# Performance work log

Hardware: AMD Instinct MI355X
Metric: run time of the kernel (lower is better)

The kernel has to match this reference:

```python
import jax, jax.numpy as jnp
import numpy as np

V, D, L, H, T_BLK, DFF = 50257, 768, 12, 12, 1024, 4096
DK = D // H
LN_EPS = 1e-5


def setup_inputs() -> dict:
    key = jax.random.key(0)
    ks = jax.random.split(key, 16)
    s = 0.02
    inp = {
        "idx": jax.random.randint(ks[0], (2, 1024), 0, V),
        "tok_emb": jax.random.normal(ks[1], (V, D), jnp.float32) * s,
        "pos_emb": jax.random.normal(ks[2], (1, T_BLK, D), jnp.float32) * s,
        "ln1_w": jnp.ones((L, D), jnp.float32),
        "ln1_b": jnp.zeros((L, D), jnp.float32),
        "qkv_w": jax.random.normal(ks[3], (L, 3 * D, D), jnp.float32) * s,
        "qkv_b": jnp.zeros((L, 3 * D), jnp.float32),
        "proj_w": jax.random.normal(ks[4], (L, D, D), jnp.float32) * s,
        "proj_b": jnp.zeros((L, D), jnp.float32),
        "ln2_w": jnp.ones((L, D), jnp.float32),
        "ln2_b": jnp.zeros((L, D), jnp.float32),
        "ff1_w": jax.random.normal(ks[5], (L, DFF, D), jnp.float32) * s,
        "ff1_b": jnp.zeros((L, DFF), jnp.float32),
        "ff2_w": jax.random.normal(ks[6], (L, D, DFF), jnp.float32) * s,
        "ff2_b": jnp.zeros((L, D), jnp.float32),
        "lnf_w": jnp.ones((D,), jnp.float32),
        "lnf_b": jnp.zeros((D,), jnp.float32),
        "head_w": jax.random.normal(ks[7], (V, D), jnp.float32) * s,
    }
    return inp


def _layernorm(x, w, b):
    mu = jnp.mean(x, axis=-1, keepdims=True)
    var = jnp.var(x, axis=-1, keepdims=True)
    return (x - mu) * jax.lax.rsqrt(var + LN_EPS) * w + b


def _gpt_forward(idx, tok_emb, pos_emb, ln1_w, ln1_b, qkv_w, qkv_b, proj_w, proj_b,
                 ln2_w, ln2_b, ff1_w, ff1_b, ff2_w, ff2_b, lnf_w, lnf_b, head_w):
    B, T = idx.shape
    x = tok_emb[idx] + pos_emb[:, :T, :]  # [B,T,D]
    mask = jnp.tril(jnp.ones((T, T), bool))  # causal
    scale = 1.0 / np.sqrt(DK)

    def step(x, p):
        l1w, l1b, qw, qb, pw, pb, l2w, l2b, f1w, f1b, f2w, f2b = p
        h = _layernorm(x, l1w, l1b)
        qkv = h @ qw.T + qb  # [B,T,3D]
        q, k, v = jnp.split(qkv, 3, axis=-1)
        q = q.reshape(B, T, H, DK).transpose(0, 2, 1, 3)  # [B,H,T,DK]
        k = k.reshape(B, T, H, DK).transpose(0, 2, 1, 3)
        v = v.reshape(B, T, H, DK).transpose(0, 2, 1, 3)
        att = jnp.einsum('bhtd,bhsd->bhts', q, k) * scale
        att = jnp.where(mask, att, -jnp.inf)
        att = jax.nn.softmax(att, axis=-1)
        y = jnp.einsum('bhts,bhsd->bhtd', att, v)
        y = y.transpose(0, 2, 1, 3).reshape(B, T, D)
        x = x + y @ pw.T + pb
        h2 = _layernorm(x, l2w, l2b)
        ff = jax.nn.gelu(h2 @ f1w.T + f1b, approximate=False) @ f2w.T + f2b
        return x + ff, None

    params = (ln1_w, ln1_b, qkv_w, qkv_b, proj_w, proj_b,
              ln2_w, ln2_b, ff1_w, ff1_b, ff2_w, ff2_b)
    x, _ = jax.lax.scan(step, x, params)
    x = _layernorm(x, lnf_w, lnf_b)
    return x @ head_w.T  # [B,T,V] logits


def reference(idx, tok_emb, pos_emb, ln1_w, ln1_b, qkv_w, qkv_b, proj_w, proj_b,
              ln2_w, ln2_b, ff1_w, ff1_b, ff2_w, ff2_b, lnf_w, lnf_b, head_w):
    return _gpt_forward(idx, tok_emb, pos_emb, ln1_w, ln1_b, qkv_w, qkv_b, proj_w,
                        proj_b, ln2_w, ln2_b, ff1_w, ff1_b, ff2_w, ff2_b,
                        lnf_w, lnf_b, head_w)
```

## Files before the change

kernel.cpp:

```cpp
#include <hip/hip_runtime.h>
#include <hip/hip_bf16.h>
#include <math.h>

#define Dm 768
#define Tt 1024
#define Bb 2
#define Hh 12
#define DFF 4096
#define Ll 12
#define Vv 50257
#define ROWS (Bb*Tt)
#define LN_EPS 1e-5f

typedef unsigned int uint;
typedef unsigned short ushort;
typedef float f32x4 __attribute__((ext_vector_type(4)));
typedef short bf16x8 __attribute__((ext_vector_type(8)));
typedef ushort us8 __attribute__((ext_vector_type(8)));

__device__ __forceinline__ ushort f2bf(float f) {
  uint u = __builtin_bit_cast(uint, f);
  u += 0x7FFFu + ((u >> 16) & 1u);
  return (ushort)(u >> 16);
}

#define GLL(gp, lp)                                                          \
  __builtin_amdgcn_global_load_lds(                                          \
      (const __attribute__((address_space(1))) uint*)(gp),                   \
      (__attribute__((address_space(3))) uint*)(lp), 16, 0, 0)

__global__ __launch_bounds__(256) void embed_ln(
    const int* __restrict__ idx, const float* __restrict__ tok,
    const float* __restrict__ pos, const float* __restrict__ w,
    const float* __restrict__ b, float* __restrict__ x,
    ushort* __restrict__ out) {
  const int row = blockIdx.x;
  const int t = row & (Tt - 1);
  const int tid = threadIdx.x;
  const float* tsrc = tok + (size_t)idx[row] * Dm;
  const float* psrc = pos + (size_t)t * Dm;
  float v[3];
  float sum = 0.f, sq = 0.f;
#pragma unroll
  for (int i = 0; i < 3; i++) {
    const int d = tid + i * 256;
    v[i] = tsrc[d] + psrc[d];
    x[(size_t)row * Dm + d] = v[i];
    sum += v[i]; sq += v[i] * v[i];
  }
#pragma unroll
  for (int off = 32; off > 0; off >>= 1) {
    sum += __shfl_xor(sum, off);
    sq  += __shfl_xor(sq, off);
  }
  __shared__ float red[8];
  const int wid = tid >> 6, lane = tid & 63;
  if (lane == 0) { red[wid] = sum; red[wid + 4] = sq; }
  __syncthreads();
  sum = red[0] + red[1] + red[2] + red[3];
  sq  = red[4] + red[5] + red[6] + red[7];
  const float mu = sum * (1.f / Dm);
  const float var = sq * (1.f / Dm) - mu * mu;
  const float rstd = rsqrtf(var + LN_EPS);
  ushort* dst = out + (size_t)row * Dm;
#pragma unroll
  for (int i = 0; i < 3; i++) {
    const int d = tid + i * 256;
    dst[d] = f2bf((v[i] - mu) * rstd * w[d] + b[d]);
  }
}

__global__ __launch_bounds__(256) void red_ln(
    const float* __restrict__ part, int nsk, const float* __restrict__ bias,
    float* __restrict__ x, const float* __restrict__ w,
    const float* __restrict__ b, ushort* __restrict__ out) {
  const int row = blockIdx.x;
  const int tid = threadIdx.x;
  float v[3];
  float sum = 0.f, sq = 0.f;
#pragma unroll
  for (int i = 0; i < 3; i++) {
    const int d = tid + i * 256;
    const size_t off = (size_t)row * Dm + d;
    float s = x[off] + bias[d];
    for (int k = 0; k < nsk; k++) s += part[(size_t)k * ROWS * Dm + off];
    x[off] = s;
    v[i] = s;
    sum += s; sq += s * s;
  }
#pragma unroll
  for (int off = 32; off > 0; off >>= 1) {
    sum += __shfl_xor(sum, off);
    sq  += __shfl_xor(sq, off);
  }
  __shared__ float red[8];
  const int wid = tid >> 6, lane = tid & 63;
  if (lane == 0) { red[wid] = sum; red[wid + 4] = sq; }
  __syncthreads();
  sum = red[0] + red[1] + red[2] + red[3];
  sq  = red[4] + red[5] + red[6] + red[7];
  const float mu = sum * (1.f / Dm);
  const float var = sq * (1.f / Dm) - mu * mu;
  const float rstd = rsqrtf(var + LN_EPS);
  ushort* dst = out + (size_t)row * Dm;
#pragma unroll
  for (int i = 0; i < 3; i++) {
    const int d = tid + i * 256;
    dst[d] = f2bf((v[i] - mu) * rstd * w[d] + b[d]);
  }
}

__global__ __launch_bounds__(256) void convert_w(
    const float* __restrict__ s, ushort* __restrict__ d, int n4) {
  const int stride = gridDim.x * 256;
  for (int i = blockIdx.x * 256 + threadIdx.x; i < n4; i += stride) {
    const float4 v = ((const float4*)s)[i];
    ushort4 o;
    o.x = f2bf(v.x); o.y = f2bf(v.y); o.z = f2bf(v.z); o.w = f2bf(v.w);
    ((ushort4*)d)[i] = o;
  }
}

#define EPI_QKV 0
#define EPI_PART 1
#define EPI_BIAS_GELU 2
#define EPI_NONE 3

template <int EPI>
__global__ __launch_bounds__(256) void gemm_mfma(
    const ushort* __restrict__ A, const ushort* __restrict__ B,
    const float* __restrict__ bias, void* __restrict__ Cv,
    void* __restrict__ Cv2, int Kloop, int Kstr, int Nloc, int ldC) {
  __shared__ char lds[32768];
  const int tid = threadIdx.x;
  const int l = tid & 63;
  const int wid = __builtin_amdgcn_readfirstlane(tid >> 6);
  const int wr = wid >> 1, wc = wid & 1;
  const int m0 = blockIdx.y * 128;
  const int n0 = blockIdx.x * 128;
  const int z = (EPI == EPI_PART) ? blockIdx.z : 0;
  if (EPI == EPI_PART) { A += (size_t)z * Kloop; B += (size_t)z * Kloop; }

  const int cperm = (((l & 3) ^ ((l >> 3) & 3)) * 8);
  const ushort* gA = A + (size_t)(m0 + wid * 32 + (l >> 2)) * Kstr + cperm;
  int rB = n0 + wid * 32 + (l >> 2);
  rB = min(rB, Nloc - 1);
  const ushort* gB = B + (size_t)rB * Kstr + cperm;

  const int rdSw = (l & 15) * 64 + (((l >> 4) ^ ((l >> 1) & 3)) * 16);
  const int aRd = wr * 4096 + rdSw;
  const int bRd = 8192 + wc * 4096 + rdSw;

  f32x4 acc[4][4] = {};
  const int nt = Kloop / 32;

  {
    const int lb = wid * 2048;
    GLL(gA, lds + lb);          GLL(gA + 16 * Kstr, lds + lb + 1024);
    GLL(gB, lds + 8192 + lb);   GLL(gB + 16 * Kstr, lds + 8192 + lb + 1024);
  }

  for (int t = 0; t < nt; ++t) {
    __syncthreads();
    if (t + 1 < nt) {
      const int base = ((t + 1) & 1) * 16384;
      const int lb = base + wid * 2048;
      const ushort* a = gA + (t + 1) * 32;
      const ushort* b = gB + (t + 1) * 32;
      GLL(a, lds + lb);         GLL(a + 16 * Kstr, lds + lb + 1024);
      GLL(b, lds + 8192 + lb);  GLL(b + 16 * Kstr, lds + 8192 + lb + 1024);
    }
    const int base = (t & 1) * 16384;
    bf16x8 av[4], bv[4];
#pragma unroll
    for (int i = 0; i < 4; ++i) {
      av[i] = *(const bf16x8*)(lds + base + aRd + i * 1024);
      bv[i] = *(const bf16x8*)(lds + base + bRd + i * 1024);
    }
#pragma unroll
    for (int i = 0; i < 4; ++i)
#pragma unroll
      for (int j = 0; j < 4; ++j)
        acc[i][j] = __builtin_amdgcn_mfma_f32_16x16x32_bf16(
            av[i], bv[j], acc[i][j], 0, 0, 0);
  }

#pragma unroll
  for (int fm = 0; fm < 4; ++fm) {
    const int row0 = m0 + wr * 64 + fm * 16 + (l >> 4) * 4;
#pragma unroll
    for (int fn = 0; fn < 4; ++fn) {
      const int col = n0 + wc * 64 + fn * 16 + (l & 15);
      if (col >= Nloc) continue;
      float bi = 0.f;
      if (EPI == EPI_QKV || EPI == EPI_BIAS_GELU) bi = bias[col];
      if (EPI == EPI_QKV && col >= 2 * Dm) {
        const int hh = (col - 2 * Dm) >> 6, dd = col & 63;
        const int bI = row0 >> 10, t0 = row0 & (Tt - 1);
        ushort4 o4;
        o4.x = f2bf(acc[fm][fn][0] + bi);
        o4.y = f2bf(acc[fm][fn][1] + bi);
        o4.z = f2bf(acc[fm][fn][2] + bi);
        o4.w = f2bf(acc[fm][fn][3] + bi);
        *(ushort4*)((ushort*)Cv2 +
                    ((size_t)((bI * Hh + hh) * 64 + dd)) * Tt + t0) = o4;
        continue;
      }
#pragma unroll
      for (int r = 0; r < 4; ++r) {
        float v = acc[fm][fn][r] + bi;
        const size_t off = (size_t)(row0 + r) * ldC + col;
        if (EPI == EPI_BIAS_GELU) {
          v = 0.5f * v * (1.f + erff(v * 0.70710678118654752f));
          ((ushort*)Cv)[off] = f2bf(v);
        } else if (EPI == EPI_QKV) {
          ((ushort*)Cv)[off] = f2bf(v);
        } else if (EPI == EPI_PART) {
          ((float*)Cv)[(size_t)z * ROWS * ldC + off] = v;
        } else {
          ((float*)Cv)[off] = v;
        }
      }
    }
  }
}

__global__ __launch_bounds__(512, 2) void gemm_head8(
    const ushort* __restrict__ A, const ushort* __restrict__ B,
    float* __restrict__ C) {
  __shared__ char lds[131072];
  const int tid = threadIdx.x;
  const int l = tid & 63;
  const int wid = __builtin_amdgcn_readfirstlane(tid >> 6);
  const int wm = wid >> 2, wn = wid & 3;

  const int bid = blockIdx.x;
  const int swz = (bid & 7) * 197 + (bid >> 3);
  const int pan = swz >> 3, mrw = swz & 7;
  const int m0 = mrw * 256;
  const int n0 = pan * 256;

  const ushort* gA[2];
  const ushort* gB[2];
#pragma unroll
  for (int j = 0; j < 2; j++) {
    const int c = tid + j * 512;
    const int r = c >> 2, kq = c & 3;
    gA[j] = A + (size_t)(m0 + r) * Dm + ((kq ^ ((r >> 1) & 3)) * 8);
    int rb = n0 + r;
    rb = min(rb, Vv - 1);
    gB[j] = B + (size_t)rb * Dm + ((kq ^ ((r >> 1) & 3)) * 8);
  }

#define HSTAGE(t)                                                            \
  do {                                                                       \
    char* _lb = lds + ((t) & 3) * 32768;                                     \
    const int _o = (t) * 32;                                                 \
    GLL(gA[0] + _o, _lb + tid * 16);                                         \
    GLL(gA[1] + _o, _lb + 8192 + tid * 16);                                  \
    GLL(gB[0] + _o, _lb + 16384 + tid * 16);                                 \
    GLL(gB[1] + _o, _lb + 24576 + tid * 16);                                 \
  } while (0)

  f32x4 acc[8][4] = {};
  const int s = l & 15, g = l >> 4;

  int aOff[8], bOff[4];
#pragma unroll
  for (int fm = 0; fm < 8; fm++) {
    const int r = wm * 128 + fm * 16 + s;
    aOff[fm] = r * 64 + ((g ^ ((r >> 1) & 3)) * 16);
  }
#pragma unroll
  for (int fn = 0; fn < 4; fn++) {
    const int r = wn * 64 + fn * 16 + s;
    bOff[fn] = 16384 + r * 64 + ((g ^ ((r >> 1) & 3)) * 16);
  }

  HSTAGE(0); HSTAGE(1); HSTAGE(2);
  asm volatile("s_waitcnt vmcnt(8)" ::: "memory");
  __builtin_amdgcn_s_barrier();
  __builtin_amdgcn_sched_barrier(0);

#define HITER(t, VC)                                                         \
  {                                                                          \
    if ((t) + 3 < 24) HSTAGE((t) + 3);                                       \
    char* bb = lds + ((t) & 3) * 32768;                                      \
    bf16x8 av[8], bv[4];                                                     \
    _Pragma("unroll")                                                        \
    for (int fm = 0; fm < 8; fm++) av[fm] = *(const bf16x8*)(bb + aOff[fm]); \
    _Pragma("unroll")                                                        \
    for (int fn = 0; fn < 4; fn++) bv[fn] = *(const bf16x8*)(bb + bOff[fn]); \
    __builtin_amdgcn_s_setprio(1);                                           \
    _Pragma("unroll")                                                        \
    for (int fm = 0; fm < 8; fm++)                                           \
      _Pragma("unroll")                                                      \
      for (int fn = 0; fn < 4; fn++)                                         \
        acc[fm][fn] = __builtin_amdgcn_mfma_f32_16x16x32_bf16(               \
            av[fm], bv[fn], acc[fm][fn], 0, 0, 0);                           \
    __builtin_amdgcn_s_setprio(0);                                           \
    asm volatile("s_waitcnt lgkmcnt(0)" ::: "memory");                       \
    asm volatile("s_waitcnt vmcnt(" #VC ")" ::: "memory");                   \
    __builtin_amdgcn_s_barrier();                                            \
    __builtin_amdgcn_sched_barrier(0);                                       \
  }

#pragma unroll 1
  for (int t = 0; t <= 20; ++t) HITER(t, 8);
  HITER(21, 4);
  HITER(22, 0);
  HITER(23, 0);

#pragma unroll
  for (int fm = 0; fm < 8; ++fm) {
    const int row0 = m0 + wm * 128 + fm * 16 + g * 4;
#pragma unroll
    for (int fn = 0; fn < 4; ++fn) {
      const int col = n0 + wn * 64 + fn * 16 + s;
      if (col >= Vv) continue;
#pragma unroll
      for (int r = 0; r < 4; ++r)
        C[(size_t)(row0 + r) * Vv + col] = acc[fm][fn][r];
    }
  }
}

__global__ __launch_bounds__(128) void attn_mfma(
    const ushort* __restrict__ qkv, const ushort* __restrict__ vTg,
    ushort* __restrict__ y) {
  __shared__ char lds[36864];
  const int tid = threadIdx.x;
  const int l = tid & 63;
  const int w = tid >> 6;
  const int s = l & 15, g = l >> 4;
  const int bq = gridDim.x - 1 - blockIdx.x;
  const int h = blockIdx.y, b = blockIdx.z;
  const int bh = b * Hh + h;

  const int qrow = bq * 32 + w * 16 + s;
  const ushort* qp = qkv + (size_t)(b * Tt + qrow) * 2304 + h * 64 + g * 8;
  const bf16x8 aq0 = *(const bf16x8*)qp;
  const bf16x8 aq1 = *(const bf16x8*)(qp + 32);

  size_t gofs[8];
#pragma unroll
  for (int i = 0; i < 8; i++) {
    const int c = tid + i * 128;
    if (i < 4) {
      const int kr = c >> 3;
      gofs[i] = (size_t)(b * Tt + kr) * 2304 + Dm + h * 64 + ((c & 7) ^ (kr & 7)) * 8;
    } else {
      const int cv = c - 512;
      const int vr = cv >> 3;
      gofs[i] = (size_t)(bh * 64 + vr) * Tt + ((cv & 7) ^ (vr & 7)) * 8;
    }
  }

#define ASTAGE(kt, base)                                                     \
  do {                                                                       \
    _Pragma("unroll")                                                        \
    for (int i = 0; i < 8; i++) {                                            \
      const ushort* p = (i < 4) ? (qkv + gofs[i] + (size_t)(kt) * 147456)    \
                                : (vTg + gofs[i] + (kt) * 64);               \
      GLL(p, lds + (base) + tid * 16 + i * 2048);                            \
    }                                                                        \
  } while (0)

  f32x4 oc[4] = {};
  float mrun[4], lrun[4];
#pragma unroll
  for (int r = 0; r < 4; r++) { mrun[r] = -INFINITY; lrun[r] = 0.f; }

  const int pB = 32768 + w * 2048;
  const int kSw = (s & 7);
  const int nkt = (bq >> 1) + 1;

  ASTAGE(0, 0);
  for (int kt = 0; kt < nkt; ++kt) {
    __syncthreads();
    if (kt + 1 < nkt) ASTAGE(kt + 1, ((kt + 1) & 1) * 16384);
    const int cur = (kt & 1) * 16384;

    f32x4 sc[4];
    __builtin_amdgcn_s_setprio(1);
#pragma unroll
    for (int jn = 0; jn < 4; jn++) {
      const int krow = cur + (jn * 16 + s) * 128;
      const bf16x8 bk0 = *(const bf16x8*)(lds + krow + ((g ^ kSw) * 16));
      const bf16x8 bk1 = *(const bf16x8*)(lds + krow + (((4 + g) ^ kSw) * 16));
      f32x4 z = {};
      z = __builtin_amdgcn_mfma_f32_16x16x32_bf16(aq0, bk0, z, 0, 0, 0);
      z = __builtin_amdgcn_mfma_f32_16x16x32_bf16(aq1, bk1, z, 0, 0, 0);
      sc[jn] = z;
    }
    __builtin_amdgcn_s_setprio(0);

    float cr[4];
    const bool diag = (kt == nkt - 1);
#pragma unroll
    for (int r = 0; r < 4; r++) {
      const int rowg = bq * 32 + w * 16 + g * 4 + r;
      float v[4];
#pragma unroll
      for (int jn = 0; jn < 4; jn++) {
        v[jn] = sc[jn][r] * 0.125f;
        if (diag && (kt * 64 + jn * 16 + s) > rowg) v[jn] = -INFINITY;
      }
      float mx = fmaxf(fmaxf(v[0], v[1]), fmaxf(v[2], v[3]));
      mx = fmaxf(mx, __shfl_xor(mx, 1));
      mx = fmaxf(mx, __shfl_xor(mx, 2));
      mx = fmaxf(mx, __shfl_xor(mx, 4));
      mx = fmaxf(mx, __shfl_xor(mx, 8));
      const float mnew = fmaxf(mrun[r], mx);
      const float corr = __expf(mrun[r] - mnew);
      mrun[r] = mnew;
      float ps = 0.f;
#pragma unroll
      for (int jn = 0; jn < 4; jn++) {
        const float p = __expf(v[jn] - mnew);
        ps += p;
        *(ushort*)(lds + pB + (g * 4 + r) * 128 +
                   (((2 * jn + (s >> 3)) ^ g) * 16) + (s & 7) * 2) = f2bf(p);
      }
      ps += __shfl_xor(ps, 1);
      ps += __shfl_xor(ps, 2);
      ps += __shfl_xor(ps, 4);
      ps += __shfl_xor(ps, 8);
      lrun[r] = lrun[r] * corr + ps;
      cr[r] = corr;
    }

    const float c01 = (s & 1) ? cr[1] : cr[0];
    const float c23 = (s & 1) ? cr[3] : cr[2];
    const float csel = (s & 2) ? c23 : c01;
    const float ccol = __shfl(csel, ((s >> 2) << 4) | s);
#pragma unroll
    for (int fm = 0; fm < 4; fm++) {
      oc[fm][0] *= ccol; oc[fm][1] *= ccol;
      oc[fm][2] *= ccol; oc[fm][3] *= ccol;
    }

    const bf16x8 bp0 = *(const bf16x8*)(lds + pB + s * 128 + ((g ^ (s >> 2)) * 16));
    const bf16x8 bp1 = *(const bf16x8*)(lds + pB + s * 128 + (((4 + g) ^ (s >> 2)) * 16));
    __builtin_amdgcn_s_setprio(1);
#pragma unroll
    for (int fm = 0; fm < 4; fm++) {
      const int vrow = cur + 8192 + (fm * 16 + s) * 128;
      const bf16x8 av0 = *(const bf16x8*)(lds + vrow + ((g ^ kSw) * 16));
      const bf16x8 av1 = *(const bf16x8*)(lds + vrow + (((4 + g) ^ kSw) * 16));
      oc[fm] = __builtin_amdgcn_mfma_f32_16x16x32_bf16(av0, bp0, oc[fm], 0, 0, 0);
      oc[fm] = __builtin_amdgcn_mfma_f32_16x16x32_bf16(av1, bp1, oc[fm], 0, 0, 0);
    }
    __builtin_amdgcn_s_setprio(0);
  }

  float li[4];
#pragma unroll
  for (int r = 0; r < 4; r++) li[r] = 1.f / lrun[r];
  const float l01 = (s & 1) ? li[1] : li[0];
  const float l23 = (s & 1) ? li[3] : li[2];
  const float lsel = (s & 2) ? l23 : l01;
  const float lcol = __shfl(lsel, ((s >> 2) << 4) | s);
  ushort* yp = y + (size_t)(b * Tt + qrow) * Dm + h * 64;
#pragma unroll
  for (int fm = 0; fm < 4; fm++) {
    ushort4 o4;
    o4.x = f2bf(oc[fm][0] * lcol);
    o4.y = f2bf(oc[fm][1] * lcol);
    o4.z = f2bf(oc[fm][2] * lcol);
    o4.w = f2bf(oc[fm][3] * lcol);
    *(ushort4*)(yp + fm * 16 + g * 4) = o4;
  }
}

extern "C" void kernel_launch(void* const* d_in, const int* in_sizes, int n_in,
                              void* d_out, int out_size, void* d_ws, size_t ws_size,
                              hipStream_t stream) {
  const int* idx = (const int*)d_in[0];
  const float* tok = (const float*)d_in[1];
  const float* pos = (const float*)d_in[2];
  const float* ln1w = (const float*)d_in[3];
  const float* ln1b = (const float*)d_in[4];
  const float* qkvw = (const float*)d_in[5];
  const float* qkvb = (const float*)d_in[6];
  const float* projw = (const float*)d_in[7];
  const float* projb = (const float*)d_in[8];
  const float* ln2w = (const float*)d_in[9];
  const float* ln2b = (const float*)d_in[10];
  const float* ff1w = (const float*)d_in[11];
  const float* ff1b = (const float*)d_in[12];
  const float* ff2w = (const float*)d_in[13];
  const float* ff2b = (const float*)d_in[14];
  const float* lnfw = (const float*)d_in[15];
  const float* lnfb = (const float*)d_in[16];
  const float* headw = (const float*)d_in[17];
  float* out = (float*)d_out;

  char* ws = (char*)d_ws;
  ushort* h    = (ushort*)ws;
  float*  x    = (float*)(ws + 3145728);
  ushort* y    = (ushort*)(ws + 9437184);
  ushort* qkv  = (ushort*)(ws + 12582912);
  ushort* vTg  = (ushort*)(ws + 22020096);
  ushort* ff   = (ushort*)(ws + 25165824);
  ushort* wb   = (ushort*)(ws + 41943040);
  float* projPart = (float*)(ws + 12582912);
  float* ff2Part  = (float*)(ws + 9437184);

  const size_t oPROJ = (size_t)Ll * 3 * Dm * Dm;
  const size_t oFF1  = oPROJ + (size_t)Ll * Dm * Dm;
  const size_t oFF2  = oFF1 + (size_t)Ll * DFF * Dm;
  const size_t oHEAD = oFF2 + (size_t)Ll * Dm * DFF;

  convert_w<<<2048, 256, 0, stream>>>(qkvw, wb, (int)(oPROJ / 4));
  convert_w<<<2048, 256, 0, stream>>>(projw, wb + oPROJ, (int)((oFF1 - oPROJ) / 4));
  convert_w<<<2048, 256, 0, stream>>>(ff1w, wb + oFF1, (int)((oFF2 - oFF1) / 4));
  convert_w<<<2048, 256, 0, stream>>>(ff2w, wb + oFF2, (int)((oHEAD - oFF2) / 4));
  convert_w<<<2048, 256, 0, stream>>>(headw, wb + oHEAD, (int)((size_t)Vv * Dm / 4));

  embed_ln<<<ROWS, 256, 0, stream>>>(idx, tok, pos, ln1w, ln1b, x, h);

  for (int l = 0; l < Ll; l++) {
    gemm_mfma<EPI_QKV><<<dim3(18, 16), 256, 0, stream>>>(
        h, wb + (size_t)l * 3 * Dm * Dm, qkvb + l * 3 * Dm, qkv, vTg,
        Dm, Dm, 3 * Dm, 3 * Dm);
    attn_mfma<<<dim3(32, Hh, Bb), 128, 0, stream>>>(qkv, vTg, y);
    gemm_mfma<EPI_PART><<<dim3(6, 16, 2), 256, 0, stream>>>(
        y, wb + oPROJ + (size_t)l * Dm * Dm, nullptr, projPart, nullptr,
        Dm / 2, Dm, Dm, Dm);
    red_ln<<<ROWS, 256, 0, stream>>>(projPart, 2, projb + l * Dm, x,
                                     ln2w + l * Dm, ln2b + l * Dm, h);
    gemm_mfma<EPI_BIAS_GELU><<<dim3(32, 16), 256, 0, stream>>>(
        h, wb + oFF1 + (size_t)l * DFF * Dm, ff1b + l * DFF, ff, nullptr,
        Dm, Dm, DFF, DFF);
    gemm_mfma<EPI_PART><<<dim3(6, 16, 2), 256, 0, stream>>>(
        ff, wb + oFF2 + (size_t)l * Dm * DFF, nullptr, ff2Part, nullptr,
        DFF / 2, DFF, Dm, Dm);
    const float* nw = (l == Ll - 1) ? lnfw : ln1w + (l + 1) * Dm;
    const float* nb = (l == Ll - 1) ? lnfb : ln1b + (l + 1) * Dm;
    red_ln<<<ROWS, 256, 0, stream>>>(ff2Part, 2, ff2b + l * Dm, x, nw, nb, h);
  }

  gemm_head8<<<1576, 512, 0, stream>>>(h, wb + oHEAD, out);
}
```

Before: 2.218 ms.

## Convert fp32 layer weights to bf16 inside GEMM loads instead of pre-pass

Removes the separate fp32-to-bf16 conversion pass over all layer weights. The GEMM kernel now reads fp32 weight tiles into registers one stage ahead, packs them to bf16 and writes them swizzled into LDS, while activations still use direct global-to-LDS loads. Only the head weight is still pre-converted. This saves a full read and write of the weights, but each GEMM now reads twice the weight bytes and spends extra register and VALU work on packing. The old clamp on B rows against Nloc is dropped.

```diff
diff --git a/kernel.cpp b/kernel.cpp
--- a/kernel.cpp
+++ b/kernel.cpp
@@ -22,6 +22,15 @@
   uint u = __builtin_bit_cast(uint, f);
   u += 0x7FFFu + ((u >> 16) & 1u);
   return (ushort)(u >> 16);
+}
+
+__device__ __forceinline__ bf16x8 pack8(f32x4 a, f32x4 b) {
+  bf16x8 o;
+  o[0] = (short)f2bf(a[0]); o[1] = (short)f2bf(a[1]);
+  o[2] = (short)f2bf(a[2]); o[3] = (short)f2bf(a[3]);
+  o[4] = (short)f2bf(b[0]); o[5] = (short)f2bf(b[1]);
+  o[6] = (short)f2bf(b[2]); o[7] = (short)f2bf(b[3]);
+  return o;
 }
 
 #define GLL(gp, lp)                                                          \
@@ -128,7 +137,7 @@
 
 template <int EPI>
 __global__ __launch_bounds__(256) void gemm_mfma(
-    const ushort* __restrict__ A, const ushort* __restrict__ B,
+    const ushort* __restrict__ A, const float* __restrict__ Bf,
     const float* __restrict__ bias, void* __restrict__ Cv,
     void* __restrict__ Cv2, int Kloop, int Kstr, int Nloc, int ldC) {
   __shared__ char lds[32768];
@@ -139,13 +148,17 @@
   const int m0 = blockIdx.y * 128;
   const int n0 = blockIdx.x * 128;
   const int z = (EPI == EPI_PART) ? blockIdx.z : 0;
-  if (EPI == EPI_PART) { A += (size_t)z * Kloop; B += (size_t)z * Kloop; }
+  if (EPI == EPI_PART) { A += (size_t)z * Kloop; Bf += (size_t)z * Kloop; }
 
   const int cperm = (((l & 3) ^ ((l >> 3) & 3)) * 8);
   const ushort* gA = A + (size_t)(m0 + wid * 32 + (l >> 2)) * Kstr + cperm;
-  int rB = n0 + wid * 32 + (l >> 2);
-  rB = min(rB, Nloc - 1);
-  const ushort* gB = B + (size_t)rB * Kstr + cperm;
+
+  const int r0 = tid >> 2, s0 = tid & 3;
+  const int q0 = s0 ^ ((r0 >> 1) & 3);
+  const float* gB0 = Bf + (size_t)(n0 + r0) * Kstr + q0 * 8;
+  const float* gB1 = Bf + (size_t)(n0 + r0 + 64) * Kstr + q0 * 8;
+  const int wOff0 = 8192 + r0 * 64 + s0 * 16;
+  const int wOff1 = 8192 + (r0 + 64) * 64 + s0 * 16;
 
   const int rdSw = (l & 15) * 64 + (((l >> 4) ^ ((l >> 1) & 3)) * 16);
   const int aRd = wr * 4096 + rdSw;
@@ -154,21 +167,32 @@
   f32x4 acc[4][4] = {};
   const int nt = Kloop / 32;
 
+  f32x4 rb0, rb1, rb2, rb3;
+  rb0 = *(const f32x4*)(gB0);     rb1 = *(const f32x4*)(gB0 + 4);
+  rb2 = *(const f32x4*)(gB1);     rb3 = *(const f32x4*)(gB1 + 4);
+  *(bf16x8*)(lds + wOff0) = pack8(rb0, rb1);
+  *(bf16x8*)(lds + wOff1) = pack8(rb2, rb3);
   {
     const int lb = wid * 2048;
-    GLL(gA, lds + lb);          GLL(gA + 16 * Kstr, lds + lb + 1024);
-    GLL(gB, lds + 8192 + lb);   GLL(gB + 16 * Kstr, lds + 8192 + lb + 1024);
-  }
+    GLL(gA, lds + lb);  GLL(gA + 16 * Kstr, lds + lb + 1024);
+  }
+  rb0 = *(const f32x4*)(gB0 + 32); rb1 = *(const f32x4*)(gB0 + 36);
+  rb2 = *(const f32x4*)(gB1 + 32); rb3 = *(const f32x4*)(gB1 + 36);
 
   for (int t = 0; t < nt; ++t) {
     __syncthreads();
     if (t + 1 < nt) {
-      const int base = ((t + 1) & 1) * 16384;
-      const int lb = base + wid * 2048;
+      char* bb = lds + ((t + 1) & 1) * 16384;
+      *(bf16x8*)(bb + wOff0) = pack8(rb0, rb1);
+      *(bf16x8*)(bb + wOff1) = pack8(rb2, rb3);
+      const int lb = ((t + 1) & 1) * 16384 + wid * 2048;
       const ushort* a = gA + (t + 1) * 32;
-      const ushort* b = gB + (t + 1) * 32;
-      GLL(a, lds + lb);         GLL(a + 16 * Kstr, lds + lb + 1024);
-      GLL(b, lds + 8192 + lb);  GLL(b + 16 * Kstr, lds + 8192 + lb + 1024);
+      GLL(a, lds + lb);  GLL(a + 16 * Kstr, lds + lb + 1024);
+    }
+    if (t + 2 < nt) {
+      const int o = (t + 2) * 32;
+      rb0 = *(const f32x4*)(gB0 + o);      rb1 = *(const f32x4*)(gB0 + o + 4);
+      rb2 = *(const f32x4*)(gB1 + o);      rb3 = *(const f32x4*)(gB1 + o + 4);
     }
     const int base = (t & 1) * 16384;
     bf16x8 av[4], bv[4];
@@ -507,39 +531,30 @@
   float* projPart = (float*)(ws + 12582912);
   float* ff2Part  = (float*)(ws + 9437184);
 
-  const size_t oPROJ = (size_t)Ll * 3 * Dm * Dm;
-  const size_t oFF1  = oPROJ + (size_t)Ll * Dm * Dm;
-  const size_t oFF2  = oFF1 + (size_t)Ll * DFF * Dm;
-  const size_t oHEAD = oFF2 + (size_t)Ll * Dm * DFF;
-
-  convert_w<<<2048, 256, 0, stream>>>(qkvw, wb, (int)(oPROJ / 4));
-  convert_w<<<2048, 256, 0, stream>>>(projw, wb + oPROJ, (int)((oFF1 - oPROJ) / 4));
-  convert_w<<<2048, 256, 0, stream>>>(ff1w, wb + oFF1, (int)((oFF2 - oFF1) / 4));
-  convert_w<<<2048, 256, 0, stream>>>(ff2w, wb + oFF2, (int)((oHEAD - oFF2) / 4));
-  convert_w<<<2048, 256, 0, stream>>>(headw, wb + oHEAD, (int)((size_t)Vv * Dm / 4));
+  convert_w<<<2048, 256, 0, stream>>>(headw, wb, (int)((size_t)Vv * Dm / 4));
 
   embed_ln<<<ROWS, 256, 0, stream>>>(idx, tok, pos, ln1w, ln1b, x, h);
 
   for (int l = 0; l < Ll; l++) {
     gemm_mfma<EPI_QKV><<<dim3(18, 16), 256, 0, stream>>>(
-        h, wb + (size_t)l * 3 * Dm * Dm, qkvb + l * 3 * Dm, qkv, vTg,
+        h, qkvw + (size_t)l * 3 * Dm * Dm, qkvb + l * 3 * Dm, qkv, vTg,
         Dm, Dm, 3 * Dm, 3 * Dm);
     attn_mfma<<<dim3(32, Hh, Bb), 128, 0, stream>>>(qkv, vTg, y);
     gemm_mfma<EPI_PART><<<dim3(6, 16, 2), 256, 0, stream>>>(
-        y, wb + oPROJ + (size_t)l * Dm * Dm, nullptr, projPart, nullptr,
+        y, projw + (size_t)l * Dm * Dm, nullptr, projPart, nullptr,
         Dm / 2, Dm, Dm, Dm);
     red_ln<<<ROWS, 256, 0, stream>>>(projPart, 2, projb + l * Dm, x,
                                      ln2w + l * Dm, ln2b + l * Dm, h);
     gemm_mfma<EPI_BIAS_GELU><<<dim3(32, 16), 256, 0, stream>>>(
-        h, wb + oFF1 + (size_t)l * DFF * Dm, ff1b + l * DFF, ff, nullptr,
+        h, ff1w + (size_t)l * DFF * Dm, ff1b + l * DFF, ff, nullptr,
         Dm, Dm, DFF, DFF);
     gemm_mfma<EPI_PART><<<dim3(6, 16, 2), 256, 0, stream>>>(
-        ff, wb + oFF2 + (size_t)l * Dm * DFF, nullptr, ff2Part, nullptr,
+        ff, ff2w + (size_t)l * Dm * DFF, nullptr, ff2Part, nullptr,
         DFF / 2, DFF, Dm, Dm);
     const float* nw = (l == Ll - 1) ? lnfw : ln1w + (l + 1) * Dm;
     const float* nb = (l == Ll - 1) ? lnfb : ln1b + (l + 1) * Dm;
     red_ln<<<ROWS, 256, 0, stream>>>(ff2Part, 2, ff2b + l * Dm, x, nw, nb, h);
   }
 
-  gemm_head8<<<1576, 512, 0, stream>>>(h, wb + oHEAD, out);
-}
+  gemm_head8<<<1576, 512, 0, stream>>>(h, wb, out);
+}
```

Measured after the change: 2.558 ms. +15.4%, slower.
